# Optimization experiments

Measured on AMD Instinct MI355X. Metric: run time of the kernel, lower is better.

Reference implementation:

```python
import jax, jax.numpy as jnp
import numpy as np

N_NODES = 50000   # nodes per channel
N_EDGES = 800000  # intra edges per channel (avg degree ~16)
N_GRAPHS = 64     # graphs in the batch (global_add_pool segments)
D = 128           # node_features_len == out_channels
L = 3             # n_layers
BN_EPS = 1e-5
NEG_SLOPE = 0.01  # F.leaky_relu default


def setup_inputs() -> dict:
    key = jax.random.key(0)
    ks = jax.random.split(key, 24)
    s = 0.05
    inp = {
        "x1": jax.random.normal(ks[0], (N_NODES, D), jnp.float32),
        "x2": jax.random.normal(ks[1], (N_NODES, D), jnp.float32),
        # GIN MLP channel 1: Linear-BN-ReLU-Linear-ReLU, stacked over layers
        "W1_ch1": jax.random.normal(ks[2], (L, D, D), jnp.float32) * s,
        "b1_ch1": jax.random.normal(ks[3], (L, D), jnp.float32) * s,
        "bn_g": 1.0 + jax.random.normal(ks[4], (L, D), jnp.float32) * s,
        "bn_b": jax.random.normal(ks[5], (L, D), jnp.float32) * s,
        "bn_m": jax.random.normal(ks[6], (L, D), jnp.float32) * s,
        "bn_v": 0.5 + jax.random.uniform(ks[7], (L, D), jnp.float32),
        "W2_ch1": jax.random.normal(ks[8], (L, D, D), jnp.float32) * s,
        "b2_ch1": jax.random.normal(ks[9], (L, D), jnp.float32) * s,
        # GIN MLP channel 2: Linear-ReLU-Linear
        "W1_ch2": jax.random.normal(ks[10], (L, D, D), jnp.float32) * s,
        "b1_ch2": jax.random.normal(ks[11], (L, D), jnp.float32) * s,
        "W2_ch2": jax.random.normal(ks[12], (L, D, D), jnp.float32) * s,
        "b2_ch2": jax.random.normal(ks[13], (L, D), jnp.float32) * s,
        # head: Linear(2*D*L -> D) - ReLU - Dropout - Linear(D -> 1)
        "Wf1": jax.random.normal(ks[14], (2 * D * L, D), jnp.float32) * s,
        "bf1": jax.random.normal(ks[15], (D,), jnp.float32) * s,
        "Wf2": jax.random.normal(ks[16], (D, 1), jnp.float32) * s,
        "bf2": jax.random.normal(ks[17], (1,), jnp.float32) * s,
        "edge1": jax.random.randint(ks[18], (2, N_EDGES), 0, N_NODES, dtype=jnp.int32),
        "edge2": jax.random.randint(ks[19], (2, N_EDGES), 0, N_NODES, dtype=jnp.int32),
        "batch1": jnp.sort(jax.random.randint(ks[20], (N_NODES,), 0, N_GRAPHS, dtype=jnp.int32)),
        "batch2": jnp.sort(jax.random.randint(ks[21], (N_NODES,), 0, N_GRAPHS, dtype=jnp.int32)),
    }
    return inp


def _aggregate(x, edge):
    # GINConv sum aggregation: message x[src] scattered to dst; eps=0 default
    return jax.ops.segment_sum(x[edge[0]], edge[1], num_segments=N_NODES)


def _channel1(x, edge, batch, W1, b1, g, b, m, v, W2, b2):
    pooled = []
    for i in range(L):
        h = (x + _aggregate(x, edge)) @ W1[i] + b1[i]
        h = (h - m[i]) * (g[i] / jnp.sqrt(v[i] + BN_EPS)) + b[i]  # eval-mode BN
        h = jax.nn.relu(h)
        h = jax.nn.relu(h @ W2[i] + b2[i])
        x = jax.nn.leaky_relu(h, NEG_SLOPE)
        pooled.append(jax.ops.segment_sum(x, batch, num_segments=N_GRAPHS))
    return jnp.concatenate(pooled, axis=-1)  # [G, D*L]


def _channel2(x, edge, batch, W1, b1, W2, b2):
    pooled = []
    for i in range(L):
        h = jax.nn.relu((x + _aggregate(x, edge)) @ W1[i] + b1[i])
        h = h @ W2[i] + b2[i]
        x = jax.nn.leaky_relu(h, NEG_SLOPE)
        pooled.append(jax.ops.segment_sum(x, batch, num_segments=N_GRAPHS))
    return jnp.concatenate(pooled, axis=-1)  # [G, D*L]


def reference(x1, x2, W1_ch1, b1_ch1, bn_g, bn_b, bn_m, bn_v, W2_ch1, b2_ch1,
              W1_ch2, b1_ch2, W2_ch2, b2_ch2, Wf1, bf1, Wf2, bf2,
              edge1, edge2, batch1, batch2):
    p1 = _channel1(x1, edge1, batch1, W1_ch1, b1_ch1, bn_g, bn_b, bn_m, bn_v, W2_ch1, b2_ch1)
    p2 = _channel2(x2, edge2, batch2, W1_ch2, b1_ch2, W2_ch2, b2_ch2)
    z = jnp.concatenate([p1, p2], axis=-1)  # [G, 2*D*L]
    h = jax.nn.relu(z @ Wf1 + bf1)          # dropout is identity in eval mode
    return h @ Wf2 + bf2                    # [G, 1]
```

## Files before the change

### kernel.cpp

```cpp
#include <hip/hip_runtime.h>

#define NN 50000
#define NE 800000
#define NG 64
#define DD 128
#define NL 3
#define ZW (2 * DD * NL)
#define NB2 128
#define NPB 391
#define CAP2 8192
#define CHUNK 4096
#define P1B 196
#define GB2 1024

typedef __attribute__((ext_vector_type(8))) short short8;
typedef __attribute__((ext_vector_type(4))) float f32x4;

__device__ inline unsigned short f2bf(float f) {
  unsigned int u = __float_as_uint(f);
  unsigned int r = (u + 0x7fffu + ((u >> 16) & 1u)) >> 16;
  return (unsigned short)r;
}

__global__ __launch_bounds__(256) void cvt_bf16_kernel(const float* __restrict__ in,
                                                       unsigned short* __restrict__ out, int n8) {
  int i = blockIdx.x * 256 + threadIdx.x;
  if (i >= n8) return;
  const float4* in4 = reinterpret_cast<const float4*>(in);
  float4 a = in4[2 * i], b = in4[2 * i + 1];
  uint4 o;
  o.x = (unsigned int)f2bf(a.x) | ((unsigned int)f2bf(a.y) << 16);
  o.y = (unsigned int)f2bf(a.z) | ((unsigned int)f2bf(a.w) << 16);
  o.z = (unsigned int)f2bf(b.x) | ((unsigned int)f2bf(b.y) << 16);
  o.w = (unsigned int)f2bf(b.z) | ((unsigned int)f2bf(b.w) << 16);
  reinterpret_cast<uint4*>(out)[i] = o;
}

__global__ __launch_bounds__(256) void cvt_wt_kernel(const float* __restrict__ in,
                                                     unsigned short* __restrict__ out) {
  __shared__ float tile[32][33];
  int mat = blockIdx.z;
  int k0 = blockIdx.x * 32, c0 = blockIdx.y * 32;
  int tx = threadIdx.x & 31, ty = threadIdx.x >> 5;
  const float* ip = in + mat * 16384;
  unsigned short* op = out + mat * 16384;
#pragma unroll
  for (int rr = 0; rr < 32; rr += 8)
    tile[ty + rr][tx] = ip[(k0 + ty + rr) * 128 + (c0 + tx)];
  __syncthreads();
#pragma unroll
  for (int rr = 0; rr < 32; rr += 8)
    op[(c0 + ty + rr) * 128 + (k0 + tx)] = f2bf(tile[tx][ty + rr]);
}

__global__ __launch_bounds__(256) void bucket_kernel(const int* __restrict__ e1,
                                                     const int* __restrict__ e2,
                                                     int* __restrict__ bcur,
                                                     uint2* __restrict__ pairs) {
  int ch = blockIdx.x >= P1B;
  int blk = blockIdx.x - ch * P1B;
  const int* E = ch ? e2 : e1;
  int base = blk * CHUNK;
  __shared__ int lcnt[NB2], gbase[NB2];
  for (int i = threadIdx.x; i < NB2; i += 256) lcnt[i] = 0;
  __syncthreads();
  int srcv[16], dstv[16], lrank[16];
#pragma unroll
  for (int k = 0; k < 16; k++) {
    int e = base + k * 256 + threadIdx.x;
    if (e < NE) {
      srcv[k] = E[e];
      dstv[k] = E[NE + e];
      lrank[k] = atomicAdd(&lcnt[dstv[k] / NPB], 1);
    } else dstv[k] = -1;
  }
  __syncthreads();
  for (int i = threadIdx.x; i < NB2; i += 256)
    gbase[i] = atomicAdd(&bcur[ch * NB2 + i], lcnt[i]);
  __syncthreads();
#pragma unroll
  for (int k = 0; k < 16; k++)
    if (dstv[k] >= 0) {
      int g = dstv[k] / NPB;
      pairs[(size_t)(ch * NB2 + g) * CAP2 + gbase[g] + lrank[k]] =
          make_uint2((unsigned)srcv[k], (unsigned)dstv[k]);
    }
}

__global__ __launch_bounds__(256) void scan_bcur_kernel(const int* __restrict__ bcur,
                                                        int* __restrict__ colbase) {
  __shared__ int s[256];
  int tid = threadIdx.x;
  int v = bcur[tid];
  s[tid] = v;
  __syncthreads();
  int segstart = tid & ~127;
  for (int o = 1; o < 128; o <<= 1) {
    int t = (tid - o >= segstart) ? s[tid - o] : 0;
    __syncthreads();
    s[tid] += t;
    __syncthreads();
  }
  colbase[tid] = s[tid] - v;
}

__global__ __launch_bounds__(256) void csr_build_kernel(const uint2* __restrict__ pairs,
                                                        const int* __restrict__ bcur,
                                                        const int* __restrict__ colbase,
                                                        int* __restrict__ rowptr,
                                                        int* __restrict__ col) {
  int g = blockIdx.x;
  int ch = g >> 7, b = g & 127;
  int node0 = b * NPB;
  int nloc = min(NPB, NN - node0);
  int count = bcur[g];
  int base = colbase[g];
  const uint2* p = pairs + (size_t)g * CAP2;
  __shared__ int hist[512], pref[512], cur[512], stmp[256];
  for (int i = threadIdx.x; i < 512; i += 256) hist[i] = 0;
  __syncthreads();
  for (int e = threadIdx.x; e < count; e += 256)
    atomicAdd(&hist[(int)p[e].y - node0], 1);
  __syncthreads();
  int t = threadIdx.x;
  int a0 = hist[2 * t], a1 = hist[2 * t + 1];
  int sum = a0 + a1;
  stmp[t] = sum;
  __syncthreads();
  for (int o = 1; o < 256; o <<= 1) {
    int tv = (t >= o) ? stmp[t - o] : 0;
    __syncthreads();
    stmp[t] += tv;
    __syncthreads();
  }
  int ex = stmp[t] - sum;
  pref[2 * t] = ex;       pref[2 * t + 1] = ex + a0;
  cur[2 * t] = ex;        cur[2 * t + 1] = ex + a0;
  __syncthreads();
  for (int i = threadIdx.x; i < nloc; i += 256)
    rowptr[ch * (NN + 1) + node0 + i] = base + pref[i];
  if (threadIdx.x == 0 && b == NB2 - 1) rowptr[ch * (NN + 1) + NN] = base + count;
  for (int e = threadIdx.x; e < count; e += 256) {
    uint2 pr = p[e];
    int pos = atomicAdd(&cur[(int)pr.y - node0], 1);
    col[ch * NE + base + pos] = (int)pr.x;
  }
}

__global__ __launch_bounds__(256) void gstart_kernel(const int* __restrict__ batch1,
                                                     const int* __restrict__ batch2,
                                                     int* __restrict__ gstart) {
  int t = threadIdx.x;
  if (t >= 2 * (NG + 1)) return;
  int ch = t / (NG + 1), g = t % (NG + 1);
  const int* b = ch ? batch2 : batch1;
  int lo = 0, hi = NN;
  while (lo < hi) {
    int m = (lo + hi) >> 1;
    if (b[m] < g) lo = m + 1; else hi = m;
  }
  gstart[t] = lo;
}

__global__ __launch_bounds__(256) void agg_kernel(const unsigned short* __restrict__ X,
                                                  const int* __restrict__ rowptr,
                                                  const int* __restrict__ col,
                                                  unsigned short* __restrict__ Y) {
  int node = blockIdx.x * 16 + (threadIdx.x >> 4);
  int lane = threadIdx.x & 15;
  int ch = node >= NN;
  int nl = node - ch * NN;
  const int* rp = rowptr + ch * (NN + 1);
  const int* cl = col + ch * NE;
  const uint4* X4 = reinterpret_cast<const uint4*>(X);
  size_t chbase = (size_t)ch * NN * 16;
  float acc[8];
  {
    uint4 sv = X4[(size_t)node * 16 + lane];
    unsigned int w[4] = {sv.x, sv.y, sv.z, sv.w};
#pragma unroll
    for (int q = 0; q < 4; q++) {
      acc[2 * q]     = __uint_as_float(w[q] << 16);
      acc[2 * q + 1] = __uint_as_float(w[q] & 0xffff0000u);
    }
  }
  int s = rp[nl], e = rp[nl + 1];
  int j = s;
  for (; j + 8 <= e; j += 8) {
    uint4 v[8];
#pragma unroll
    for (int q = 0; q < 8; q++)
      v[q] = X4[chbase + (size_t)cl[j + q] * 16 + lane];
#pragma unroll
    for (int q = 0; q < 8; q++) {
      unsigned int w[4] = {v[q].x, v[q].y, v[q].z, v[q].w};
#pragma unroll
      for (int t = 0; t < 4; t++) {
        acc[2 * t]     += __uint_as_float(w[t] << 16);
        acc[2 * t + 1] += __uint_as_float(w[t] & 0xffff0000u);
      }
    }
  }
  for (; j < e; ++j) {
    uint4 v = X4[chbase + (size_t)cl[j] * 16 + lane];
    unsigned int w[4] = {v.x, v.y, v.z, v.w};
#pragma unroll
    for (int t = 0; t < 4; t++) {
      acc[2 * t]     += __uint_as_float(w[t] << 16);
      acc[2 * t + 1] += __uint_as_float(w[t] & 0xffff0000u);
    }
  }
  uint4 o;
  unsigned int* ow = reinterpret_cast<unsigned int*>(&o);
#pragma unroll
  for (int q = 0; q < 4; q++)
    ow[q] = (unsigned int)f2bf(acc[2 * q]) | ((unsigned int)f2bf(acc[2 * q + 1]) << 16);
  reinterpret_cast<uint4*>(Y)[(size_t)node * 16 + lane] = o;
}

__global__ __launch_bounds__(256) void gemm_fused_kernel(
    const unsigned short* __restrict__ Y, unsigned short* __restrict__ X,
    const unsigned short* __restrict__ WT,
    const float* __restrict__ b1c1, const float* __restrict__ b1c2,
    const float* __restrict__ b2c1, const float* __restrict__ b2c2,
    const float* __restrict__ bng, const float* __restrict__ bnb,
    const float* __restrict__ bnm, const float* __restrict__ bnv, int layer) {
  __shared__ unsigned short hlds[16][136];
  int ch = blockIdx.x >= GB2;
  int lane = threadIdx.x & 63, wv = threadIdx.x >> 6;
  int l15 = lane & 15, lk = lane >> 4;
  int c0 = wv * 32;
  const unsigned short* W1 = WT + (size_t)(ch * 6 + layer) * 16384;
  const unsigned short* W2 = WT + (size_t)(ch * 6 + 3 + layer) * 16384;
  short8 w1f[2][4], w2f[2][4];
#pragma unroll
  for (int ct = 0; ct < 2; ct++)
#pragma unroll
    for (int kk = 0; kk < 4; kk++) {
      size_t boff = (size_t)(c0 + ct * 16 + l15) * 128 + kk * 32 + lk * 8;
      w1f[ct][kk] = *reinterpret_cast<const short8*>(W1 + boff);
      w2f[ct][kk] = *reinterpret_cast<const short8*>(W2 + boff);
    }
  const float* b1 = (ch ? b1c2 : b1c1) + layer * DD;
  const float* b2 = (ch ? b2c2 : b2c1) + layer * DD;
  float sc1[2], sh1[2], sh2[2];
#pragma unroll
  for (int ct = 0; ct < 2; ct++) {
    int colg = c0 + ct * 16 + l15;
    if (!ch) {
      float s = bng[layer * DD + colg] * rsqrtf(bnv[layer * DD + colg] + 1e-5f);
      sc1[ct] = s;
      sh1[ct] = (b1[colg] - bnm[layer * DD + colg]) * s + bnb[layer * DD + colg];
    } else {
      sc1[ct] = 1.f;
      sh1[ct] = b1[colg];
    }
    sh2[ct] = b2[colg];
  }
  for (int t = (ch ? blockIdx.x - GB2 : blockIdx.x); t < 3125; t += GB2) {
    int r0l = t * 16;
    size_t r0g = (size_t)ch * NN + r0l;
    const unsigned short* yp = Y + (r0g + l15) * 128 + lk * 8;
    short8 a0 = *reinterpret_cast<const short8*>(yp);
    short8 a1 = *reinterpret_cast<const short8*>(yp + 32);
    short8 a2 = *reinterpret_cast<const short8*>(yp + 64);
    short8 a3 = *reinterpret_cast<const short8*>(yp + 96);
#pragma unroll
    for (int ct = 0; ct < 2; ct++) {
      f32x4 acc = {0.f, 0.f, 0.f, 0.f};
      acc = __builtin_amdgcn_mfma_f32_16x16x32_bf16(a0, w1f[ct][0], acc, 0, 0, 0);
      acc = __builtin_amdgcn_mfma_f32_16x16x32_bf16(a1, w1f[ct][1], acc, 0, 0, 0);
      acc = __builtin_amdgcn_mfma_f32_16x16x32_bf16(a2, w1f[ct][2], acc, 0, 0, 0);
      acc = __builtin_amdgcn_mfma_f32_16x16x32_bf16(a3, w1f[ct][3], acc, 0, 0, 0);
      int colg = c0 + ct * 16 + l15;
#pragma unroll
      for (int r = 0; r < 4; r++) {
        float tv = fmaxf(acc[r] * sc1[ct] + sh1[ct], 0.f);
        hlds[lk * 4 + r][colg] = f2bf(tv);
      }
    }
    __syncthreads();
    short8 h0 = *reinterpret_cast<const short8*>(&hlds[l15][lk * 8]);
    short8 h1 = *reinterpret_cast<const short8*>(&hlds[l15][32 + lk * 8]);
    short8 h2 = *reinterpret_cast<const short8*>(&hlds[l15][64 + lk * 8]);
    short8 h3 = *reinterpret_cast<const short8*>(&hlds[l15][96 + lk * 8]);
#pragma unroll
    for (int ct = 0; ct < 2; ct++) {
      f32x4 acc = {0.f, 0.f, 0.f, 0.f};
      acc = __builtin_amdgcn_mfma_f32_16x16x32_bf16(h0, w2f[ct][0], acc, 0, 0, 0);
      acc = __builtin_amdgcn_mfma_f32_16x16x32_bf16(h1, w2f[ct][1], acc, 0, 0, 0);
      acc = __builtin_amdgcn_mfma_f32_16x16x32_bf16(h2, w2f[ct][2], acc, 0, 0, 0);
      acc = __builtin_amdgcn_mfma_f32_16x16x32_bf16(h3, w2f[ct][3], acc, 0, 0, 0);
      int colg = c0 + ct * 16 + l15;
#pragma unroll
      for (int r = 0; r < 4; r++) {
        float tv = acc[r] + sh2[ct];
        if (!ch) tv = fmaxf(tv, 0.f);
        else     tv = tv > 0.f ? tv : 0.01f * tv;
        X[(r0g + lk * 4 + r) * 128 + colg] = f2bf(tv);
      }
    }
    __syncthreads();
  }
}

__global__ __launch_bounds__(256) void pool_kernel(const unsigned short* __restrict__ X,
                                                   const int* __restrict__ gstart,
                                                   float* __restrict__ z, int layer) {
  int ch = blockIdx.x >> 6, g = blockIdx.x & 63;
  int r0 = gstart[ch * (NG + 1) + g], r1 = gstart[ch * (NG + 1) + g + 1];
  int c8 = threadIdx.x & 15, part = threadIdx.x >> 4;
  const uint4* X4 = reinterpret_cast<const uint4*>(X);
  size_t base = (size_t)ch * NN * 16 + c8;
  float acc[8];
#pragma unroll
  for (int q = 0; q < 8; q++) acc[q] = 0.f;
  int r = r0 + part;
  for (; r + 48 < r1; r += 64) {
    uint4 v0 = X4[base + (size_t)r * 16];
    uint4 v1 = X4[base + (size_t)(r + 16) * 16];
    uint4 v2 = X4[base + (size_t)(r + 32) * 16];
    uint4 v3 = X4[base + (size_t)(r + 48) * 16];
    unsigned int w0[4] = {v0.x, v0.y, v0.z, v0.w};
    unsigned int w1[4] = {v1.x, v1.y, v1.z, v1.w};
    unsigned int w2[4] = {v2.x, v2.y, v2.z, v2.w};
    unsigned int w3[4] = {v3.x, v3.y, v3.z, v3.w};
#pragma unroll
    for (int q = 0; q < 4; q++) {
      acc[2 * q]     += __uint_as_float(w0[q] << 16) + __uint_as_float(w1[q] << 16) +
                        __uint_as_float(w2[q] << 16) + __uint_as_float(w3[q] << 16);
      acc[2 * q + 1] += __uint_as_float(w0[q] & 0xffff0000u) + __uint_as_float(w1[q] & 0xffff0000u) +
                        __uint_as_float(w2[q] & 0xffff0000u) + __uint_as_float(w3[q] & 0xffff0000u);
    }
  }
  for (; r < r1; r += 16) {
    uint4 v = X4[base + (size_t)r * 16];
    unsigned int w[4] = {v.x, v.y, v.z, v.w};
#pragma unroll
    for (int q = 0; q < 4; q++) {
      acc[2 * q]     += __uint_as_float(w[q] << 16);
      acc[2 * q + 1] += __uint_as_float(w[q] & 0xffff0000u);
    }
  }
  __shared__ float zacc[16][128];
#pragma unroll
  for (int q = 0; q < 8; q++) zacc[part][c8 * 8 + q] = acc[q];
  __syncthreads();
  for (int s = 8; s > 0; s >>= 1) {
    if (part < s) {
#pragma unroll
      for (int q = 0; q < 8; q++)
        zacc[part][c8 * 8 + q] += zacc[part + s][c8 * 8 + q];
    }
    __syncthreads();
  }
  if (part == 0) {
#pragma unroll
    for (int q = 0; q < 8; q++) {
      int colw = c8 * 8 + q;
      z[(size_t)g * ZW + ch * DD * NL + layer * DD + colw] = zacc[0][colw];
    }
  }
}

__global__ __launch_bounds__(128) void head_kernel(const float* __restrict__ z,
                                                   const float* __restrict__ Wf1,
                                                   const float* __restrict__ bf1,
                                                   const float* __restrict__ Wf2,
                                                   const float* __restrict__ bf2,
                                                   float* __restrict__ out) {
  int g = blockIdx.x, t = threadIdx.x;
  const float* zr = z + (size_t)g * ZW;
  float acc = bf1[t];
  for (int j = 0; j < ZW; ++j) acc += zr[j] * Wf1[(size_t)j * DD + t];
  float h = fmaxf(acc, 0.f);
  __shared__ float red[128];
  red[t] = h * Wf2[t];
  __syncthreads();
  for (int s = 64; s > 0; s >>= 1) {
    if (t < s) red[t] += red[t + s];
    __syncthreads();
  }
  if (t == 0) out[g] = red[0] + bf2[0];
}

extern "C" void kernel_launch(void* const* d_in, const int* in_sizes, int n_in,
                              void* d_out, int out_size, void* d_ws, size_t ws_size,
                              hipStream_t stream) {
  const float* x1   = (const float*)d_in[0];
  const float* x2   = (const float*)d_in[1];
  const float* W1c1 = (const float*)d_in[2];
  const float* b1c1 = (const float*)d_in[3];
  const float* bng  = (const float*)d_in[4];
  const float* bnb  = (const float*)d_in[5];
  const float* bnm  = (const float*)d_in[6];
  const float* bnv  = (const float*)d_in[7];
  const float* W2c1 = (const float*)d_in[8];
  const float* b2c1 = (const float*)d_in[9];
  const float* W1c2 = (const float*)d_in[10];
  const float* b1c2 = (const float*)d_in[11];
  const float* W2c2 = (const float*)d_in[12];
  const float* b2c2 = (const float*)d_in[13];
  const float* Wf1  = (const float*)d_in[14];
  const float* bf1  = (const float*)d_in[15];
  const float* Wf2  = (const float*)d_in[16];
  const float* bf2  = (const float*)d_in[17];
  const int* edge1  = (const int*)d_in[18];
  const int* edge2  = (const int*)d_in[19];
  const int* batch1 = (const int*)d_in[20];
  const int* batch2 = (const int*)d_in[21];
  (void)ws_size; (void)n_in; (void)in_sizes; (void)out_size;

  char* ws = (char*)d_ws;
  const size_t NB16 = (size_t)2 * NN * DD * 2;
  unsigned short* bufA = (unsigned short*)(ws);
  unsigned short* bufB = (unsigned short*)(ws + NB16);
  unsigned short* bufY = (unsigned short*)(ws + 2 * NB16);
  size_t off = 3 * NB16;
  unsigned short* WT = (unsigned short*)(ws + off); off += (size_t)12 * 16384 * 2;
  uint2* pairs = (uint2*)(ws + off); off += (size_t)2 * NB2 * CAP2 * 8;
  int* col     = (int*)(ws + off); off += (size_t)2 * NE * 4;
  int* rowptr  = (int*)(ws + off); off += (((size_t)2 * (NN + 1) * 4) + 255) & ~(size_t)255;
  int* bcur    = (int*)(ws + off); off += 256 * 4;
  int* colbase = (int*)(ws + off); off += 256 * 4;
  int* gstart  = (int*)(ws + off); off += 256 * 4;
  float* z     = (float*)(ws + off); off += (size_t)NG * ZW * 4;

  cvt_wt_kernel<<<dim3(4, 4, 3), 256, 0, stream>>>(W1c1, WT + 0 * 16384);
  cvt_wt_kernel<<<dim3(4, 4, 3), 256, 0, stream>>>(W2c1, WT + 3 * 16384);
  cvt_wt_kernel<<<dim3(4, 4, 3), 256, 0, stream>>>(W1c2, WT + 6 * 16384);
  cvt_wt_kernel<<<dim3(4, 4, 3), 256, 0, stream>>>(W2c2, WT + 9 * 16384);

  hipMemsetAsync(bcur, 0, 256 * 4, stream);

  cvt_bf16_kernel<<<(NN * DD / 8 + 255) / 256, 256, 0, stream>>>(x1, bufA, NN * DD / 8);
  cvt_bf16_kernel<<<(NN * DD / 8 + 255) / 256, 256, 0, stream>>>(x2, bufA + (size_t)NN * DD,
                                                                 NN * DD / 8);

  bucket_kernel<<<2 * P1B, 256, 0, stream>>>(edge1, edge2, bcur, pairs);
  scan_bcur_kernel<<<1, 256, 0, stream>>>(bcur, colbase);
  csr_build_kernel<<<2 * NB2, 256, 0, stream>>>(pairs, bcur, colbase, rowptr, col);
  gstart_kernel<<<1, 256, 0, stream>>>(batch1, batch2, gstart);

  unsigned short* cin = bufA;
  unsigned short* cout = bufB;
  for (int i = 0; i < NL; ++i) {
    agg_kernel<<<2 * NN / 16, 256, 0, stream>>>(cin, rowptr, col, bufY);
    gemm_fused_kernel<<<2 * GB2, 256, 0, stream>>>(bufY, cout, WT,
                                                   b1c1, b1c2, b2c1, b2c2,
                                                   bng, bnb, bnm, bnv, i);
    pool_kernel<<<2 * NG, 256, 0, stream>>>(cout, gstart, z, i);
    unsigned short* tmp = cin; cin = cout; cout = tmp;
  }

  head_kernel<<<NG, 128, 0, stream>>>(z, Wf1, bf1, Wf2, bf2, (float*)d_out);
}
```

Before: 388.9 us.

## Merge setup kernels, deepen gather unroll, and prefetch GEMM A tiles

Several unrelated changes land together. The four weight-transpose launches become one, as do the two x-conversion launches, and the scan and gstart kernels are merged. This is meant to cut launch overhead. The aggregation kernel now loads 16 neighbor indices and then 16 rows per iteration, with a 4-wide tail and a launch_bounds occupancy hint, to expose more memory-level parallelism in the gather. The GEMM kernel software-prefetches the next tile's A fragments to overlap global loads with MFMA work, which raises register pressure.

Measured after the change: 390.2 us. About the same (+0.3%).

```diff
diff --git a/kernel.cpp b/kernel.cpp
--- a/kernel.cpp
+++ b/kernel.cpp
@@ -2,6 +2,7 @@
 
 #define NN 50000
 #define NE 800000
+#define TOTN (2 * NN)
 #define NG 64
 #define DD 128
 #define NL 3
@@ -21,29 +22,40 @@
   unsigned int r = (u + 0x7fffu + ((u >> 16) & 1u)) >> 16;
   return (unsigned short)r;
 }
-
-__global__ __launch_bounds__(256) void cvt_bf16_kernel(const float* __restrict__ in,
-                                                       unsigned short* __restrict__ out, int n8) {
+__device__ inline float bflo(unsigned int u) { return __uint_as_float(u << 16); }
+__device__ inline float bfhi(unsigned int u) { return __uint_as_float(u & 0xffff0000u); }
+
+__global__ __launch_bounds__(256) void cvt_x_kernel(const float* __restrict__ x1,
+                                                    const float* __restrict__ x2,
+                                                    unsigned short* __restrict__ X) {
   int i = blockIdx.x * 256 + threadIdx.x;
-  if (i >= n8) return;
-  const float4* in4 = reinterpret_cast<const float4*>(in);
-  float4 a = in4[2 * i], b = in4[2 * i + 1];
+  if (i >= TOTN * DD / 8) return;
+  const int per = NN * DD / 8;
+  int ch = i >= per;
+  const float* x = ch ? x2 : x1;
+  int il = i - ch * per;
+  const float4* in4 = reinterpret_cast<const float4*>(x);
+  float4 a = in4[2 * il], b = in4[2 * il + 1];
   uint4 o;
   o.x = (unsigned int)f2bf(a.x) | ((unsigned int)f2bf(a.y) << 16);
   o.y = (unsigned int)f2bf(a.z) | ((unsigned int)f2bf(a.w) << 16);
   o.z = (unsigned int)f2bf(b.x) | ((unsigned int)f2bf(b.y) << 16);
   o.w = (unsigned int)f2bf(b.z) | ((unsigned int)f2bf(b.w) << 16);
-  reinterpret_cast<uint4*>(out)[i] = o;
-}
-
-__global__ __launch_bounds__(256) void cvt_wt_kernel(const float* __restrict__ in,
+  reinterpret_cast<uint4*>(X)[i] = o;
+}
+
+__global__ __launch_bounds__(256) void cvt_wt_kernel(const float* __restrict__ p0,
+                                                     const float* __restrict__ p1,
+                                                     const float* __restrict__ p2,
+                                                     const float* __restrict__ p3,
                                                      unsigned short* __restrict__ out) {
   __shared__ float tile[32][33];
-  int mat = blockIdx.z;
+  int slot = blockIdx.z;
+  int grp = slot / 3, mat = slot % 3;
+  const float* ip = (grp == 0 ? p0 : grp == 1 ? p1 : grp == 2 ? p2 : p3) + mat * 16384;
+  unsigned short* op = out + slot * 16384;
   int k0 = blockIdx.x * 32, c0 = blockIdx.y * 32;
   int tx = threadIdx.x & 31, ty = threadIdx.x >> 5;
-  const float* ip = in + mat * 16384;
-  unsigned short* op = out + mat * 16384;
 #pragma unroll
   for (int rr = 0; rr < 32; rr += 8)
     tile[ty + rr][tx] = ip[(k0 + ty + rr) * 128 + (c0 + tx)];
@@ -87,21 +99,37 @@
     }
 }
 
-__global__ __launch_bounds__(256) void scan_bcur_kernel(const int* __restrict__ bcur,
-                                                        int* __restrict__ colbase) {
-  __shared__ int s[256];
-  int tid = threadIdx.x;
-  int v = bcur[tid];
-  s[tid] = v;
-  __syncthreads();
-  int segstart = tid & ~127;
-  for (int o = 1; o < 128; o <<= 1) {
-    int t = (tid - o >= segstart) ? s[tid - o] : 0;
-    __syncthreads();
-    s[tid] += t;
-    __syncthreads();
-  }
-  colbase[tid] = s[tid] - v;
+__global__ __launch_bounds__(256) void scan_gstart_kernel(const int* __restrict__ bcur,
+                                                          int* __restrict__ colbase,
+                                                          const int* __restrict__ batch1,
+                                                          const int* __restrict__ batch2,
+                                                          int* __restrict__ gstart) {
+  if (blockIdx.x == 0) {
+    __shared__ int s[256];
+    int tid = threadIdx.x;
+    int v = bcur[tid];
+    s[tid] = v;
+    __syncthreads();
+    int segstart = tid & ~127;
+    for (int o = 1; o < 128; o <<= 1) {
+      int t = (tid - o >= segstart) ? s[tid - o] : 0;
+      __syncthreads();
+      s[tid] += t;
+      __syncthreads();
+    }
+    colbase[tid] = s[tid] - v;
+  } else {
+    int t = threadIdx.x;
+    if (t >= 2 * (NG + 1)) return;
+    int ch = t / (NG + 1), g = t % (NG + 1);
+    const int* b = ch ? batch2 : batch1;
+    int lo = 0, hi = NN;
+    while (lo < hi) {
+      int m = (lo + hi) >> 1;
+      if (b[m] < g) lo = m + 1; else hi = m;
+    }
+    gstart[t] = lo;
+  }
 }
 
 __global__ __launch_bounds__(256) void csr_build_kernel(const uint2* __restrict__ pairs,
@@ -147,25 +175,10 @@
   }
 }
 
-__global__ __launch_bounds__(256) void gstart_kernel(const int* __restrict__ batch1,
-                                                     const int* __restrict__ batch2,
-                                                     int* __restrict__ gstart) {
-  int t = threadIdx.x;
-  if (t >= 2 * (NG + 1)) return;
-  int ch = t / (NG + 1), g = t % (NG + 1);
-  const int* b = ch ? batch2 : batch1;
-  int lo = 0, hi = NN;
-  while (lo < hi) {
-    int m = (lo + hi) >> 1;
-    if (b[m] < g) lo = m + 1; else hi = m;
-  }
-  gstart[t] = lo;
-}
-
-__global__ __launch_bounds__(256) void agg_kernel(const unsigned short* __restrict__ X,
-                                                  const int* __restrict__ rowptr,
-                                                  const int* __restrict__ col,
-                                                  unsigned short* __restrict__ Y) {
+__global__ __launch_bounds__(256, 4) void agg_kernel(const unsigned short* __restrict__ X,
+                                                     const int* __restrict__ rowptr,
+                                                     const int* __restrict__ col,
+                                                     unsigned short* __restrict__ Y) {
   int node = blockIdx.x * 16 + (threadIdx.x >> 4);
   int lane = threadIdx.x & 15;
   int ch = node >= NN;
@@ -180,24 +193,43 @@
     unsigned int w[4] = {sv.x, sv.y, sv.z, sv.w};
 #pragma unroll
     for (int q = 0; q < 4; q++) {
-      acc[2 * q]     = __uint_as_float(w[q] << 16);
-      acc[2 * q + 1] = __uint_as_float(w[q] & 0xffff0000u);
+      acc[2 * q]     = bflo(w[q]);
+      acc[2 * q + 1] = bfhi(w[q]);
     }
   }
   int s = rp[nl], e = rp[nl + 1];
   int j = s;
-  for (; j + 8 <= e; j += 8) {
-    uint4 v[8];
-#pragma unroll
-    for (int q = 0; q < 8; q++)
-      v[q] = X4[chbase + (size_t)cl[j + q] * 16 + lane];
-#pragma unroll
-    for (int q = 0; q < 8; q++) {
+  for (; j + 16 <= e; j += 16) {
+    int idx[16];
+#pragma unroll
+    for (int q = 0; q < 16; q++) idx[q] = cl[j + q];
+    uint4 v[16];
+#pragma unroll
+    for (int q = 0; q < 16; q++) v[q] = X4[chbase + (size_t)idx[q] * 16 + lane];
+#pragma unroll
+    for (int q = 0; q < 16; q++) {
       unsigned int w[4] = {v[q].x, v[q].y, v[q].z, v[q].w};
 #pragma unroll
-      for (int t = 0; t < 4; t++) {
-        acc[2 * t]     += __uint_as_float(w[t] << 16);
-        acc[2 * t + 1] += __uint_as_float(w[t] & 0xffff0000u);
+      for (int u = 0; u < 4; u++) {
+        acc[2 * u]     += bflo(w[u]);
+        acc[2 * u + 1] += bfhi(w[u]);
+      }
+    }
+  }
+  for (; j + 4 <= e; j += 4) {
+    int idx[4];
+#pragma unroll
+    for (int q = 0; q < 4; q++) idx[q] = cl[j + q];
+    uint4 v[4];
+#pragma unroll
+    for (int q = 0; q < 4; q++) v[q] = X4[chbase + (size_t)idx[q] * 16 + lane];
+#pragma unroll
+    for (int q = 0; q < 4; q++) {
+      unsigned int w[4] = {v[q].x, v[q].y, v[q].z, v[q].w};
+#pragma unroll
+      for (int u = 0; u < 4; u++) {
+        acc[2 * u]     += bflo(w[u]);
+        acc[2 * u + 1] += bfhi(w[u]);
       }
     }
   }
@@ -205,9 +237,9 @@
     uint4 v = X4[chbase + (size_t)cl[j] * 16 + lane];
     unsigned int w[4] = {v.x, v.y, v.z, v.w};
 #pragma unroll
-    for (int t = 0; t < 4; t++) {
-      acc[2 * t]     += __uint_as_float(w[t] << 16);
-      acc[2 * t + 1] += __uint_as_float(w[t] & 0xffff0000u);
+    for (int u = 0; u < 4; u++) {
+      acc[2 * u]     += bflo(w[u]);
+      acc[2 * u + 1] += bfhi(w[u]);
     }
   }
   uint4 o;
@@ -257,14 +289,28 @@
     }
     sh2[ct] = b2[colg];
   }
-  for (int t = (ch ? blockIdx.x - GB2 : blockIdx.x); t < 3125; t += GB2) {
+  int t0 = ch ? blockIdx.x - GB2 : blockIdx.x;
+  short8 a0, a1, a2, a3;
+  {
+    size_t r0g = (size_t)ch * NN + t0 * 16;
+    const unsigned short* yp = Y + (r0g + l15) * 128 + lk * 8;
+    a0 = *reinterpret_cast<const short8*>(yp);
+    a1 = *reinterpret_cast<const short8*>(yp + 32);
+    a2 = *reinterpret_cast<const short8*>(yp + 64);
+    a3 = *reinterpret_cast<const short8*>(yp + 96);
+  }
+  for (int t = t0; t < 3125; t += GB2) {
     int r0l = t * 16;
     size_t r0g = (size_t)ch * NN + r0l;
-    const unsigned short* yp = Y + (r0g + l15) * 128 + lk * 8;
-    short8 a0 = *reinterpret_cast<const short8*>(yp);
-    short8 a1 = *reinterpret_cast<const short8*>(yp + 32);
-    short8 a2 = *reinterpret_cast<const short8*>(yp + 64);
-    short8 a3 = *reinterpret_cast<const short8*>(yp + 96);
+    short8 n0, n1, n2, n3;
+    int tn = t + GB2;
+    if (tn < 3125) {
+      const unsigned short* yp = Y + ((size_t)ch * NN + tn * 16 + l15) * 128 + lk * 8;
+      n0 = *reinterpret_cast<const short8*>(yp);
+      n1 = *reinterpret_cast<const short8*>(yp + 32);
+      n2 = *reinterpret_cast<const short8*>(yp + 64);
+      n3 = *reinterpret_cast<const short8*>(yp + 96);
+    }
 #pragma unroll
     for (int ct = 0; ct < 2; ct++) {
       f32x4 acc = {0.f, 0.f, 0.f, 0.f};
@@ -301,6 +347,7 @@
       }
     }
     __syncthreads();
+    a0 = n0; a1 = n1; a2 = n2; a3 = n3;
   }
 }
 
@@ -327,10 +374,8 @@
     unsigned int w3[4] = {v3.x, v3.y, v3.z, v3.w};
 #pragma unroll
     for (int q = 0; q < 4; q++) {
-      acc[2 * q]     += __uint_as_float(w0[q] << 16) + __uint_as_float(w1[q] << 16) +
-                        __uint_as_float(w2[q] << 16) + __uint_as_float(w3[q] << 16);
-      acc[2 * q + 1] += __uint_as_float(w0[q] & 0xffff0000u) + __uint_as_float(w1[q] & 0xffff0000u) +
-                        __uint_as_float(w2[q] & 0xffff0000u) + __uint_as_float(w3[q] & 0xffff0000u);
+      acc[2 * q]     += bflo(w0[q]) + bflo(w1[q]) + bflo(w2[q]) + bflo(w3[q]);
+      acc[2 * q + 1] += bfhi(w0[q]) + bfhi(w1[q]) + bfhi(w2[q]) + bfhi(w3[q]);
     }
   }
   for (; r < r1; r += 16) {
@@ -338,8 +383,8 @@
     unsigned int w[4] = {v.x, v.y, v.z, v.w};
 #pragma unroll
     for (int q = 0; q < 4; q++) {
-      acc[2 * q]     += __uint_as_float(w[q] << 16);
-      acc[2 * q + 1] += __uint_as_float(w[q] & 0xffff0000u);
+      acc[2 * q]     += bflo(w[q]);
+      acc[2 * q + 1] += bfhi(w[q]);
     }
   }
   __shared__ float zacc[16][128];
@@ -412,7 +457,7 @@
   (void)ws_size; (void)n_in; (void)in_sizes; (void)out_size;
 
   char* ws = (char*)d_ws;
-  const size_t NB16 = (size_t)2 * NN * DD * 2;
+  const size_t NB16 = (size_t)TOTN * DD * 2;
   unsigned short* bufA = (unsigned short*)(ws);
   unsigned short* bufB = (unsigned short*)(ws + NB16);
   unsigned short* bufY = (unsigned short*)(ws + 2 * NB16);
@@ -426,26 +471,18 @@
   int* gstart  = (int*)(ws + off); off += 256 * 4;
   float* z     = (float*)(ws + off); off += (size_t)NG * ZW * 4;
 
-  cvt_wt_kernel<<<dim3(4, 4, 3), 256, 0, stream>>>(W1c1, WT + 0 * 16384);
-  cvt_wt_kernel<<<dim3(4, 4, 3), 256, 0, stream>>>(W2c1, WT + 3 * 16384);
-  cvt_wt_kernel<<<dim3(4, 4, 3), 256, 0, stream>>>(W1c2, WT + 6 * 16384);
-  cvt_wt_kernel<<<dim3(4, 4, 3), 256, 0, stream>>>(W2c2, WT + 9 * 16384);
-
+  cvt_wt_kernel<<<dim3(4, 4, 12), 256, 0, stream>>>(W1c1, W2c1, W1c2, W2c2, WT);
   hipMemsetAsync(bcur, 0, 256 * 4, stream);
-
-  cvt_bf16_kernel<<<(NN * DD / 8 + 255) / 256, 256, 0, stream>>>(x1, bufA, NN * DD / 8);
-  cvt_bf16_kernel<<<(NN * DD / 8 + 255) / 256, 256, 0, stream>>>(x2, bufA + (size_t)NN * DD,
-                                                                 NN * DD / 8);
+  cvt_x_kernel<<<(TOTN * DD / 8 + 255) / 256, 256, 0, stream>>>(x1, x2, bufA);
 
   bucket_kernel<<<2 * P1B, 256, 0, stream>>>(edge1, edge2, bcur, pairs);
-  scan_bcur_kernel<<<1, 256, 0, stream>>>(bcur, colbase);
+  scan_gstart_kernel<<<2, 256, 0, stream>>>(bcur, colbase, batch1, batch2, gstart);
   csr_build_kernel<<<2 * NB2, 256, 0, stream>>>(pairs, bcur, colbase, rowptr, col);
-  gstart_kernel<<<1, 256, 0, stream>>>(batch1, batch2, gstart);
 
   unsigned short* cin = bufA;
   unsigned short* cout = bufB;
   for (int i = 0; i < NL; ++i) {
-    agg_kernel<<<2 * NN / 16, 256, 0, stream>>>(cin, rowptr, col, bufY);
+    agg_kernel<<<TOTN / 16, 256, 0, stream>>>(cin, rowptr, col, bufY);
     gemm_fused_kernel<<<2 * GB2, 256, 0, stream>>>(bufY, cout, WT,
                                                    b1c1, b1c2, b2c1, b2c2,
                                                    bng, bnb, bnm, bnv, i);
```
